# Kernel optimization log

Measured on AMD Instinct MI355X. Metric: run time of the kernel, lower is better.

## Reference

```python
import jax, jax.numpy as jnp
import numpy as np

B, T, K, D = 16, 1024, 8, 768
H = D // 2

def setup_inputs() -> dict:
    key = jax.random.key(0)
    ks = jax.random.split(key, 18)
    s = 0.02  # param init scale
    return {
        'emb':        jax.random.normal(ks[0], (B, T, D), jnp.float32),
        'cls_embed':  jax.random.normal(ks[1], (D,), jnp.float32),
        'Wg_w':       jax.random.normal(ks[2], (D, D), jnp.float32) * s,
        'Wg_b':       jax.random.normal(ks[3], (D,), jnp.float32) * s,
        'alpha_left': jax.random.normal(ks[4], (D,), jnp.float32),
        'alpha_right':jax.random.normal(ks[5], (D,), jnp.float32),
        'gru_Wih':    jax.random.normal(ks[6], (3 * H, D), jnp.float32) * s,
        'gru_bih':    jax.random.normal(ks[7], (3 * H,), jnp.float32) * s,
        'gru_Whh':    jax.random.normal(ks[8], (3 * H, H), jnp.float32) * s,
        'gru_bhh':    jax.random.normal(ks[9], (3 * H,), jnp.float32) * s,
        'Wc_w':       jax.random.normal(ks[10], (3, D + H), jnp.float32) * s,
        'Wc_b':       jax.random.normal(ks[11], (3,), jnp.float32) * s,
        'We_w':       jax.random.normal(ks[12], (3, D + H), jnp.float32) * s,
        'We_b':       jax.random.normal(ks[13], (3,), jnp.float32) * s,
        'child_idx':  jax.random.randint(ks[14], (B, T, K), 0, T, jnp.int32),
        'child_mask': jax.random.randint(ks[15], (B, T, K), 0, 2, jnp.int32),
        'clue_mask':  jax.random.randint(ks[16], (B, T), 0, 2, jnp.int32),
    }

def _forward(emb, cls_embed, Wg_w, Wg_b, alpha_left, alpha_right,
             gru_Wih, gru_bih, gru_Whh, gru_bhh, Wc_w, Wc_b, We_w, We_b,
             child_idx, child_mask, clue_mask):
    # ---- GAT over syntactic children (graph_attention) ----
    Wg_t = emb @ Wg_w.T + Wg_b                                  # [B,T,D] = W_g(t)
    self_score = Wg_t @ alpha_left                              # [B,T]  alpha_left . W_g(t_i)
    gather = jax.vmap(lambda w, i: w[i])                        # per-sentence child gather
    Wg_child = gather(Wg_t, child_idx)                          # [B,T,K,D]
    child_score = Wg_child @ alpha_right                        # [B,T,K]
    mask = child_mask.astype(bool)
    s = jax.nn.leaky_relu(self_score[..., None] + child_score, negative_slope=0.2)
    s = jnp.where(mask, s, -1e9)
    a = jax.nn.softmax(s, axis=-1)
    a = jnp.where(mask, a, 0.0)
    attn = jnp.einsum('btk,btkd->btd', a, Wg_child)             # a_ij @ Wg_tks
    has_child = mask.any(-1)                                    # no children -> keep t_i
    new_emb = emb + jnp.where(has_child[..., None], attn, 0.0)  # t_i' = t_i + sum

    # ---- G_W with prepended CLS row ----
    cls = jnp.broadcast_to(cls_embed, (B, 1, D))
    G_W = jnp.concatenate([cls, new_emb], axis=1)               # [B,T+1,D]
    m = jnp.concatenate([jnp.ones((B, 1), bool), clue_mask.astype(bool)], axis=1)

    # ---- GRU over clue subsequence (masked state update == packed sequence) ----
    x_proj = G_W @ gru_Wih.T + gru_bih                          # [B,T+1,3H]
    def cell(h, inp):
        xp, mt = inp                                            # [B,3H], [B]
        hp = h @ gru_Whh.T + gru_bhh
        xr, xz, xn = jnp.split(xp, 3, axis=-1)
        hr, hz, hn = jnp.split(hp, 3, axis=-1)
        r = jax.nn.sigmoid(xr + hr)
        z = jax.nn.sigmoid(xz + hz)
        n = jnp.tanh(xn + r * hn)
        h_new = (1.0 - z) * n + z * h
        h = jnp.where(mt[:, None], h_new, h)
        return h, None
    h0 = jnp.zeros((B, H), emb.dtype)
    h_clue, _ = jax.lax.scan(cell, h0, (x_proj.transpose(1, 0, 2), m.T))  # [B,H]

    # ---- cause / effect heads, drop CLS row ----
    feat = jnp.concatenate([G_W, jnp.broadcast_to(h_clue[:, None, :], (B, T + 1, H))], axis=-1)
    O_cause = (feat @ Wc_w.T + Wc_b)[:, 1:]                     # [B,T,3]
    O_effect = (feat @ We_w.T + We_b)[:, 1:]                    # [B,T,3]
    return O_cause, O_effect

def reference(emb, cls_embed, Wg_w, Wg_b, alpha_left, alpha_right,
              gru_Wih, gru_bih, gru_Whh, gru_bhh, Wc_w, Wc_b, We_w, We_b,
              child_idx, child_mask, clue_mask):
    return _forward(emb, cls_embed, Wg_w, Wg_b, alpha_left, alpha_right,
                    gru_Wih, gru_bih, gru_Whh, gru_bhh, Wc_w, Wc_b, We_w, We_b,
                    child_idx, child_mask, clue_mask)
```

## Files before the change

### kernel.cpp

```cpp
#include <hip/hip_runtime.h>
#include <hip/hip_bf16.h>
#include <math.h>

#define DD 768
#define HH 384
#define BB 16
#define TT 1024
#define NIH 1152
#define GSP 6

typedef __attribute__((ext_vector_type(8))) short short8;
typedef __attribute__((ext_vector_type(8))) __bf16 bf16x8;
typedef __attribute__((ext_vector_type(4))) float f32x4;

static __device__ __forceinline__ unsigned short f2bf(float f) {
  unsigned u = __float_as_uint(f);
  u += 0x7fffu + ((u >> 16) & 1u);
  return (unsigned short)(u >> 16);
}
static __device__ __forceinline__ float bf2f(unsigned short h) {
  return __uint_as_float(((unsigned)h) << 16);
}

__global__ void prep_convert(const float* __restrict__ wgw, const float* __restrict__ wih,
                             const float* __restrict__ whh,
                             unsigned short* __restrict__ wgw_bf, unsigned short* __restrict__ wih_bf,
                             unsigned short* __restrict__ whh_bf)
{
  const int n1 = DD*DD, n2 = NIH*DD, n3 = NIH*HH;
  int stride = gridDim.x * 256;
  for (int idx = blockIdx.x*256 + threadIdx.x; idx < n1+n2+n3; idx += stride) {
    if (idx < n1)            wgw_bf[idx]       = f2bf(wgw[idx]);
    else if (idx < n1+n2)    wih_bf[idx-n1]    = f2bf(wih[idx-n1]);
    else                     whh_bf[idx-n1-n2] = f2bf(whh[idx-n1-n2]);
  }
}

__global__ void prep_vecs(const float* __restrict__ wgw, const float* __restrict__ wgb,
                          const float* __restrict__ aL, const float* __restrict__ aR,
                          float* __restrict__ vLR, float* __restrict__ c01)
{
  int tid = threadIdx.x;
  if (blockIdx.x < 3) {
    int j = blockIdx.x*256 + tid;
    float al = 0.f, ar = 0.f;
    for (int i = 0; i < DD; ++i) { float wv = wgw[i*DD + j]; al += wv*aL[i]; ar += wv*aR[i]; }
    vLR[j] = al; vLR[DD + j] = ar;
  } else {
    float al = 0.f, ar = 0.f;
    for (int i = tid; i < DD; i += 256) { float bv = wgb[i]; al += bv*aL[i]; ar += bv*aR[i]; }
    for (int off = 32; off; off >>= 1) { al += __shfl_down(al, off); ar += __shfl_down(ar, off); }
    __shared__ float red[8];
    int w = tid >> 6, l = tid & 63;
    if (l == 0) { red[w*2] = al; red[w*2+1] = ar; }
    __syncthreads();
    if (tid == 0) { c01[0] = red[0]+red[2]+red[4]+red[6]; c01[1] = red[1]+red[3]+red[5]+red[7]; }
  }
}

__global__ __launch_bounds__(256) void scores_cvt(const float* __restrict__ emb,
    const float* __restrict__ vLR, const float* __restrict__ c01,
    float* __restrict__ ss, float* __restrict__ sr)
{
  int row = blockIdx.x, tid = threadIdx.x;
  const float* er = emb + (size_t)row*DD;
  float al = 0.f, ar = 0.f;
  for (int d = tid; d < DD; d += 256) {
    float e = er[d];
    al += e*vLR[d]; ar += e*vLR[DD+d];
  }
  for (int off = 32; off; off >>= 1) { al += __shfl_down(al, off); ar += __shfl_down(ar, off); }
  __shared__ float red[8];
  int w = tid >> 6, l = tid & 63;
  if (l == 0) { red[w*2] = al; red[w*2+1] = ar; }
  __syncthreads();
  if (tid == 0) {
    ss[row] = red[0]+red[2]+red[4]+red[6] + c01[0];
    sr[row] = red[1]+red[3]+red[5]+red[7] + c01[1];
  }
}

template<bool AF32>
__global__ __launch_bounds__(256) void gemm_bt(const void* __restrict__ Av,
    const unsigned short* __restrict__ Bw, const float* __restrict__ bias,
    unsigned short* __restrict__ C, int N, int MT, int Mreal)
{
  __shared__ __align__(16) unsigned short As[128][40];
  __shared__ __align__(16) unsigned short Bs[128][40];
  int tid = threadIdx.x;
  int tm = blockIdx.x % MT, tn = blockIdx.x / MT;
  int l = tid & 63, lr = l & 15, lk = l >> 4;
  int w = tid >> 6;
  int wm = (w >> 1)*64, wn = (w & 1)*64;
  f32x4 acc[4][4] = {};

  int c0 = tid, c1 = tid + 256;
  int r0 = c0 >> 2, ch0 = c0 & 3;
  int r1 = c1 >> 2, ch1 = c1 & 3;
  const unsigned short* Bbase = Bw + (size_t)tn*128*DD;

  for (int kt = 0; kt < 24; ++kt) {
    short8 va0, va1;
    if constexpr (AF32) {
      const float* Af = (const float*)Av + (size_t)tm*128*DD;
      f32x4 a0l = *(const f32x4*)(Af + r0*DD + kt*32 + ch0*8);
      f32x4 a0h = *(const f32x4*)(Af + r0*DD + kt*32 + ch0*8 + 4);
      f32x4 a1l = *(const f32x4*)(Af + r1*DD + kt*32 + ch1*8);
      f32x4 a1h = *(const f32x4*)(Af + r1*DD + kt*32 + ch1*8 + 4);
      #pragma unroll
      for (int j = 0; j < 4; ++j) {
        va0[j] = (short)f2bf(a0l[j]); va0[4+j] = (short)f2bf(a0h[j]);
        va1[j] = (short)f2bf(a1l[j]); va1[4+j] = (short)f2bf(a1h[j]);
      }
    } else {
      const unsigned short* Ab = (const unsigned short*)Av + (size_t)tm*128*DD;
      va0 = *(const short8*)(Ab + r0*DD + kt*32 + ch0*8);
      va1 = *(const short8*)(Ab + r1*DD + kt*32 + ch1*8);
    }
    short8 vb0 = *(const short8*)(Bbase + r0*DD + kt*32 + ch0*8);
    short8 vb1 = *(const short8*)(Bbase + r1*DD + kt*32 + ch1*8);
    __syncthreads();
    *(short8*)&As[r0][ch0*8] = va0;
    *(short8*)&As[r1][ch1*8] = va1;
    *(short8*)&Bs[r0][ch0*8] = vb0;
    *(short8*)&Bs[r1][ch1*8] = vb1;
    __syncthreads();
    bf16x8 af[4], bfr[4];
    #pragma unroll
    for (int mi = 0; mi < 4; ++mi)
      af[mi] = __builtin_bit_cast(bf16x8, *(const short8*)&As[wm + mi*16 + lr][lk*8]);
    #pragma unroll
    for (int ni = 0; ni < 4; ++ni)
      bfr[ni] = __builtin_bit_cast(bf16x8, *(const short8*)&Bs[wn + ni*16 + lr][lk*8]);
    #pragma unroll
    for (int mi = 0; mi < 4; ++mi)
      #pragma unroll
      for (int ni = 0; ni < 4; ++ni)
        acc[mi][ni] = __builtin_amdgcn_mfma_f32_16x16x32_bf16(af[mi], bfr[ni], acc[mi][ni], 0, 0, 0);
  }
  for (int mi = 0; mi < 4; ++mi) {
    int rbase = tm*128 + wm + mi*16 + lk*4;
    for (int ni = 0; ni < 4; ++ni) {
      int col = tn*128 + wn + ni*16 + lr;
      float bv = bias[col];
      #pragma unroll
      for (int jr = 0; jr < 4; ++jr) {
        int row = rbase + jr;
        if (row < Mreal) C[(size_t)row*N + col] = f2bf(acc[mi][ni][jr] + bv);
      }
    }
  }
}

__global__ __launch_bounds__(256) void gat_attn(const float* __restrict__ emb,
    const float* __restrict__ cls, const unsigned short* __restrict__ wgt_bf,
    const float* __restrict__ ss, const float* __restrict__ sr,
    const int* __restrict__ cidx, const int* __restrict__ cmask,
    unsigned short* __restrict__ gw_bf)
{
  int bx = blockIdx.x, tid = threadIdx.x;
  if (bx >= BB*TT) {
    int b = bx - BB*TT;
    unsigned short* dst = gw_bf + (size_t)(b*(TT+1))*DD;
    for (int d = tid; d < DD; d += 256) dst[d] = f2bf(cls[d]);
    return;
  }
  int b = bx >> 10, t = bx & 1023;
  __shared__ float sw[8];
  __shared__ int   si[8];
  __shared__ int   sm[8];
  if (tid < 8) {
    int ci = cidx[(size_t)bx*8 + tid];
    int cm = cmask[(size_t)bx*8 + tid];
    float s = ss[bx] + sr[(b<<10) + ci];
    s = s > 0.f ? s : 0.2f*s;
    sw[tid] = cm ? s : -1e9f;
    si[tid] = ci;
    sm[tid] = cm;
  }
  __syncthreads();
  float a[8];
  float mx = -1e30f;
  #pragma unroll
  for (int k = 0; k < 8; ++k) mx = fmaxf(mx, sw[k]);
  float sum = 0.f;
  #pragma unroll
  for (int k = 0; k < 8; ++k) { a[k] = expf(sw[k]-mx); sum += a[k]; }
  float inv = 1.f/sum;
  #pragma unroll
  for (int k = 0; k < 8; ++k) a[k] = sm[k] ? a[k]*inv : 0.f;
  const float* er = emb + (size_t)bx*DD;
  unsigned short* dst = gw_bf + (size_t)(b*(TT+1) + t + 1)*DD;
  for (int d = tid; d < DD; d += 256) {
    float acc = er[d];
    #pragma unroll
    for (int k = 0; k < 8; ++k)
      if (a[k] != 0.f) acc += a[k]*bf2f(wgt_bf[((size_t)(b<<10) + si[k])*DD + d]);
    dst[d] = f2bf(acc);
  }
}

__global__ __launch_bounds__(384, 2) void gru_scan(const unsigned short* __restrict__ whh_bf,
    const float* __restrict__ bhh, const unsigned short* __restrict__ xp,
    const int* __restrict__ clue, unsigned* __restrict__ hbuf,
    float* __restrict__ hfinal)
{
  __shared__ __align__(16) unsigned short h_bf[HH];
  __shared__ __align__(16) float y_s[192];
  __shared__ float bhh_s[192];
  __shared__ unsigned char m_s[TT+1];
  int tid = threadIdx.x;
  int b = blockIdx.x % BB, g = blockIdx.x / BB;
  int w = tid >> 6, l = tid & 63, lr = l & 15, lk = l >> 4;

  bf16x8 areg[2][12];
  #pragma unroll
  for (int i = 0; i < 2; ++i) {
    int rg = w*2 + i;
    int gate = rg >> 2;
    const unsigned short* src = whh_bf + (size_t)(gate*HH + g*64 + (rg & 3)*16 + lr)*HH;
    #pragma unroll
    for (int c = 0; c < 12; ++c) {
      int kt = 2*g + c; if (kt >= 12) kt -= 12;
      areg[i][c] = __builtin_bit_cast(bf16x8, *(const short8*)(src + kt*32 + lk*8));
    }
  }
  if (tid < 192) {
    int gate = tid / 64, e = tid % 64;
    bhh_s[tid] = bhh[gate*HH + g*64 + e];
  }
  h_bf[tid] = 0;
  for (int t = tid; t < TT; t += 384) m_s[t+1] = (clue[b*TT + t] != 0) ? 1 : 0;
  if (tid == 0) m_s[0] = 1;
  __syncthreads();

  float h_prev = 0.f;
  int gi = g*64 + tid;
  int s = 0;
  int rj = 0;
  if (tid >= 64) { int e = g*64 + 64 + (tid - 64); if (e >= HH) e -= HH; rj = e; }
  for (int t = 0; t <= TT; ++t) {
    if (!m_s[t]) continue;
    ++s;
    float xr = 0.f, xz = 0.f, xn = 0.f;
    if (tid < 64) {
      const unsigned short* xrow = xp + (size_t)(b*(TT+1) + t)*NIH;
      xr = bf2f(xrow[gi]); xz = bf2f(xrow[HH + gi]); xn = bf2f(xrow[2*HH + gi]);
    }
    f32x4 aco[2] = {};
    #pragma unroll
    for (int c = 0; c < 2; ++c) {
      bf16x8 bfr = __builtin_bit_cast(bf16x8, *(const short8*)&h_bf[g*64 + c*32 + lk*8]);
      #pragma unroll
      for (int i = 0; i < 2; ++i)
        aco[i] = __builtin_amdgcn_mfma_f32_16x16x32_bf16(areg[i][c], bfr, aco[i], 0, 0, 0);
    }
    if (s > 1 && tid >= 64) {
      const unsigned* pa = hbuf + ((size_t)(s-1)*BB + b)*HH + rj;
      unsigned tag = (unsigned)(s-1);
      unsigned v = __hip_atomic_load(pa, __ATOMIC_RELAXED, __HIP_MEMORY_SCOPE_AGENT);
      while ((v & 0xFFFFu) != tag)
        v = __hip_atomic_load(pa, __ATOMIC_RELAXED, __HIP_MEMORY_SCOPE_AGENT);
      h_bf[rj] = (unsigned short)(v >> 16);
    }
    __syncthreads();
    f32x4 acA[2] = {}, acB[2] = {};
    #pragma unroll
    for (int c = 2; c < 7; ++c) {
      int kk = g*64 + c*32; if (kk >= HH) kk -= HH;
      bf16x8 bfr = __builtin_bit_cast(bf16x8, *(const short8*)&h_bf[kk + lk*8]);
      #pragma unroll
      for (int i = 0; i < 2; ++i)
        acA[i] = __builtin_amdgcn_mfma_f32_16x16x32_bf16(areg[i][c], bfr, acA[i], 0, 0, 0);
    }
    #pragma unroll
    for (int c = 7; c < 12; ++c) {
      int kk = g*64 + c*32; if (kk >= HH) kk -= HH;
      bf16x8 bfr = __builtin_bit_cast(bf16x8, *(const short8*)&h_bf[kk + lk*8]);
      #pragma unroll
      for (int i = 0; i < 2; ++i)
        acB[i] = __builtin_amdgcn_mfma_f32_16x16x32_bf16(areg[i][c], bfr, acB[i], 0, 0, 0);
    }
    if (lr == 0) {
      #pragma unroll
      for (int i = 0; i < 2; ++i)
        *(f32x4*)&y_s[(w*2+i)*16 + lk*4] = aco[i] + acA[i] + acB[i];
    }
    __syncthreads();
    unsigned* slot = hbuf + ((size_t)s*BB + b)*HH;
    if (tid < 64) {
      float hr = y_s[tid]       + bhh_s[tid];
      float hz = y_s[64 + tid]  + bhh_s[64 + tid];
      float hn = y_s[128 + tid] + bhh_s[128 + tid];
      float rg = 1.f/(1.f + __expf(-(xr + hr)));
      float zg = 1.f/(1.f + __expf(-(xz + hz)));
      float a  = xn + rg*hn;
      a = fminf(fmaxf(a, -15.f), 15.f);
      float e2 = __expf(-2.f*a);
      float ng = (1.f - e2)/(1.f + e2);
      float hnew = (1.f - zg)*ng + zg*h_prev;
      h_prev = hnew;
      unsigned short hb16 = f2bf(hnew);
      h_bf[gi] = hb16;
      __hip_atomic_store(slot + gi, ((unsigned)hb16 << 16) | (unsigned)s,
                         __ATOMIC_RELAXED, __HIP_MEMORY_SCOPE_AGENT);
    }
    __syncthreads();
  }
  if (tid < 64) hfinal[b*HH + gi] = h_prev;
}

__global__ __launch_bounds__(384) void hpart_k(const float* __restrict__ hfinal,
    const float* __restrict__ Wc, const float* __restrict__ Wcb,
    const float* __restrict__ We, const float* __restrict__ Web, float* __restrict__ hpart)
{
  int b = blockIdx.x, tid = threadIdx.x;
  int j = tid >> 6, l = tid & 63;
  const float* wr = ((j < 3) ? (Wc + j*NIH) : (We + (j-3)*NIH)) + DD;
  float acc = 0.f;
  #pragma unroll
  for (int i = 0; i < 6; ++i) acc += hfinal[b*HH + l + i*64] * wr[l + i*64];
  for (int off = 32; off; off >>= 1) acc += __shfl_down(acc, off);
  if (l == 0) hpart[b*6 + j] = acc + ((j < 3) ? Wcb[j] : Web[j-3]);
}

__global__ __launch_bounds__(256) void heads(const unsigned short* __restrict__ gw_bf,
    const float* __restrict__ Wc, const float* __restrict__ We,
    const float* __restrict__ hpart, float* __restrict__ out)
{
  __shared__ float Wl[6][DD];
  int tid = threadIdx.x;
  for (int idx = tid; idx < 6*DD; idx += 256) {
    int j = idx / DD, d = idx % DD;
    Wl[j][d] = (j < 3) ? Wc[j*NIH + d] : We[(j-3)*NIH + d];
  }
  __syncthreads();
  int w = tid >> 6, l = tid & 63;
  int row = blockIdx.x*4 + w;
  int b = row >> 10, t = row & 1023;
  const unsigned short* gr = gw_bf + (size_t)(b*(TT+1) + t + 1)*DD;
  float acc[6] = {0,0,0,0,0,0};
  for (int i = 0; i < 12; ++i) {
    int d = l + i*64;
    float v = bf2f(gr[d]);
    #pragma unroll
    for (int j = 0; j < 6; ++j) acc[j] += v * Wl[j][d];
  }
  #pragma unroll
  for (int j = 0; j < 6; ++j)
    for (int off = 32; off; off >>= 1) acc[j] += __shfl_down(acc[j], off);
  if (l == 0) {
    const float* hp = hpart + b*6;
    float* oc = out + (size_t)b*TT*3 + t*3;
    float* oe = out + (size_t)BB*TT*3 + (size_t)b*TT*3 + t*3;
    oc[0] = acc[0]+hp[0]; oc[1] = acc[1]+hp[1]; oc[2] = acc[2]+hp[2];
    oe[0] = acc[3]+hp[3]; oe[1] = acc[4]+hp[4]; oe[2] = acc[5]+hp[5];
  }
}

extern "C" void kernel_launch(void* const* d_in, const int* in_sizes, int n_in,
                              void* d_out, int out_size, void* d_ws, size_t ws_size,
                              hipStream_t stream)
{
  const float* emb  = (const float*)d_in[0];
  const float* cls  = (const float*)d_in[1];
  const float* wgw  = (const float*)d_in[2];
  const float* wgb  = (const float*)d_in[3];
  const float* aL   = (const float*)d_in[4];
  const float* aR   = (const float*)d_in[5];
  const float* wih  = (const float*)d_in[6];
  const float* bih  = (const float*)d_in[7];
  const float* whh  = (const float*)d_in[8];
  const float* bhh  = (const float*)d_in[9];
  const float* wcw  = (const float*)d_in[10];
  const float* wcb  = (const float*)d_in[11];
  const float* wew  = (const float*)d_in[12];
  const float* web  = (const float*)d_in[13];
  const int* cidx   = (const int*)d_in[14];
  const int* cmask  = (const int*)d_in[15];
  const int* clue   = (const int*)d_in[16];
  (void)in_sizes; (void)n_in; (void)out_size; (void)ws_size;

  char* ws = (char*)d_ws;
  size_t off = 0;
  auto alloc = [&](size_t bytes) { char* p = ws + off; off += (bytes + 255) & ~(size_t)255; return p; };
  unsigned short* xp_bf  = (unsigned short*)alloc((size_t)16512*1152*2);
  unsigned short* wgt_bf = xp_bf;
  unsigned short* gw_bf  = (unsigned short*)alloc((size_t)16512*768*2);
  unsigned short* wgw_bf = (unsigned short*)alloc((size_t)768*768*2);
  unsigned short* wih_bf = (unsigned short*)alloc((size_t)1152*768*2);
  unsigned short* whh_bf = (unsigned short*)alloc((size_t)1152*384*2);
  float* vLR   = (float*)alloc(1536*4);
  float* c01   = (float*)alloc(256);
  float* ss    = (float*)alloc(16384*4);
  float* sr    = (float*)alloc(16384*4);
  unsigned* hbuf = (unsigned*)alloc((size_t)(TT+2)*BB*HH*4);
  float* hfin  = (float*)alloc((size_t)16*384*4);
  float* hpart = (float*)alloc(512);

  prep_convert<<<2048, 256, 0, stream>>>(wgw, wih, whh, wgw_bf, wih_bf, whh_bf);
  prep_vecs<<<4, 256, 0, stream>>>(wgw, wgb, aL, aR, vLR, c01);
  scores_cvt<<<16384, 256, 0, stream>>>(emb, vLR, c01, ss, sr);
  gemm_bt<true><<<128*6, 256, 0, stream>>>(emb, wgw_bf, wgb, wgt_bf, 768, 128, 16384);
  gat_attn<<<16384+16, 256, 0, stream>>>(emb, cls, wgt_bf, ss, sr, cidx, cmask, gw_bf);
  gemm_bt<false><<<129*9, 256, 0, stream>>>(gw_bf, wih_bf, bih, xp_bf, 1152, 129, 16400);
  gru_scan<<<BB*GSP, 384, 0, stream>>>(whh_bf, bhh, xp_bf, clue, hbuf, hfin);
  hpart_k<<<16, 384, 0, stream>>>(hfin, wcw, wcb, wew, web, hpart);
  heads<<<4096, 256, 0, stream>>>(gw_bf, wcw, wew, hpart, (float*)d_out);
}
```

Baseline: 839.4 us.

## Split GRU scan across 12 blocks per sequence with 32 hidden units each

```diff
diff --git a/kernel.cpp b/kernel.cpp
--- a/kernel.cpp
+++ b/kernel.cpp
@@ -7,7 +7,7 @@
 #define BB 16
 #define TT 1024
 #define NIH 1152
-#define GSP 6
+#define GSP 12
 
 typedef __attribute__((ext_vector_type(8))) short short8;
 typedef __attribute__((ext_vector_type(8))) __bf16 bf16x8;
@@ -206,28 +206,25 @@
     float* __restrict__ hfinal)
 {
   __shared__ __align__(16) unsigned short h_bf[HH];
-  __shared__ __align__(16) float y_s[192];
-  __shared__ float bhh_s[192];
+  __shared__ __align__(16) float y_s[96];
+  __shared__ float bhh_s[96];
   __shared__ unsigned char m_s[TT+1];
   int tid = threadIdx.x;
   int b = blockIdx.x % BB, g = blockIdx.x / BB;
   int w = tid >> 6, l = tid & 63, lr = l & 15, lk = l >> 4;
 
-  bf16x8 areg[2][12];
-  #pragma unroll
-  for (int i = 0; i < 2; ++i) {
-    int rg = w*2 + i;
-    int gate = rg >> 2;
-    const unsigned short* src = whh_bf + (size_t)(gate*HH + g*64 + (rg & 3)*16 + lr)*HH;
+  bf16x8 areg[12];
+  {
+    const unsigned short* src = whh_bf + (size_t)((w>>1)*HH + g*32 + (w&1)*16 + lr)*HH;
     #pragma unroll
     for (int c = 0; c < 12; ++c) {
-      int kt = 2*g + c; if (kt >= 12) kt -= 12;
-      areg[i][c] = __builtin_bit_cast(bf16x8, *(const short8*)(src + kt*32 + lk*8));
-    }
-  }
-  if (tid < 192) {
-    int gate = tid / 64, e = tid % 64;
-    bhh_s[tid] = bhh[gate*HH + g*64 + e];
+      int kt = g + c; if (kt >= 12) kt -= 12;
+      areg[c] = __builtin_bit_cast(bf16x8, *(const short8*)(src + kt*32 + lk*8));
+    }
+  }
+  if (tid < 96) {
+    int gate = tid >> 5, e = tid & 31;
+    bhh_s[tid] = bhh[gate*HH + g*32 + e];
   }
   h_bf[tid] = 0;
   for (int t = tid; t < TT; t += 384) m_s[t+1] = (clue[b*TT + t] != 0) ? 1 : 0;
@@ -235,27 +232,24 @@
   __syncthreads();
 
   float h_prev = 0.f;
-  int gi = g*64 + tid;
+  int gi = g*32 + tid;
   int s = 0;
   int rj = 0;
-  if (tid >= 64) { int e = g*64 + 64 + (tid - 64); if (e >= HH) e -= HH; rj = e; }
+  if (tid >= 32) { int e = g*32 + 32 + (tid - 32); if (e >= HH) e -= HH; rj = e; }
   for (int t = 0; t <= TT; ++t) {
     if (!m_s[t]) continue;
     ++s;
     float xr = 0.f, xz = 0.f, xn = 0.f;
-    if (tid < 64) {
+    if (tid < 32) {
       const unsigned short* xrow = xp + (size_t)(b*(TT+1) + t)*NIH;
       xr = bf2f(xrow[gi]); xz = bf2f(xrow[HH + gi]); xn = bf2f(xrow[2*HH + gi]);
     }
-    f32x4 aco[2] = {};
-    #pragma unroll
-    for (int c = 0; c < 2; ++c) {
-      bf16x8 bfr = __builtin_bit_cast(bf16x8, *(const short8*)&h_bf[g*64 + c*32 + lk*8]);
-      #pragma unroll
-      for (int i = 0; i < 2; ++i)
-        aco[i] = __builtin_amdgcn_mfma_f32_16x16x32_bf16(areg[i][c], bfr, aco[i], 0, 0, 0);
-    }
-    if (s > 1 && tid >= 64) {
+    f32x4 aco = {};
+    {
+      bf16x8 bfr = __builtin_bit_cast(bf16x8, *(const short8*)&h_bf[g*32 + lk*8]);
+      aco = __builtin_amdgcn_mfma_f32_16x16x32_bf16(areg[0], bfr, aco, 0, 0, 0);
+    }
+    if (s > 1 && tid >= 32) {
       const unsigned* pa = hbuf + ((size_t)(s-1)*BB + b)*HH + rj;
       unsigned tag = (unsigned)(s-1);
       unsigned v = __hip_atomic_load(pa, __ATOMIC_RELAXED, __HIP_MEMORY_SCOPE_AGENT);
@@ -264,34 +258,29 @@
       h_bf[rj] = (unsigned short)(v >> 16);
     }
     __syncthreads();
-    f32x4 acA[2] = {}, acB[2] = {};
-    #pragma unroll
-    for (int c = 2; c < 7; ++c) {
-      int kk = g*64 + c*32; if (kk >= HH) kk -= HH;
+    f32x4 acA = {}, acB = {};
+    #pragma unroll
+    for (int c = 1; c < 7; ++c) {
+      int kk = g*32 + c*32; if (kk >= HH) kk -= HH;
       bf16x8 bfr = __builtin_bit_cast(bf16x8, *(const short8*)&h_bf[kk + lk*8]);
-      #pragma unroll
-      for (int i = 0; i < 2; ++i)
-        acA[i] = __builtin_amdgcn_mfma_f32_16x16x32_bf16(areg[i][c], bfr, acA[i], 0, 0, 0);
+      acA = __builtin_amdgcn_mfma_f32_16x16x32_bf16(areg[c], bfr, acA, 0, 0, 0);
     }
     #pragma unroll
     for (int c = 7; c < 12; ++c) {
-      int kk = g*64 + c*32; if (kk >= HH) kk -= HH;
+      int kk = g*32 + c*32; if (kk >= HH) kk -= HH;
       bf16x8 bfr = __builtin_bit_cast(bf16x8, *(const short8*)&h_bf[kk + lk*8]);
-      #pragma unroll
-      for (int i = 0; i < 2; ++i)
-        acB[i] = __builtin_amdgcn_mfma_f32_16x16x32_bf16(areg[i][c], bfr, acB[i], 0, 0, 0);
+      acB = __builtin_amdgcn_mfma_f32_16x16x32_bf16(areg[c], bfr, acB, 0, 0, 0);
     }
     if (lr == 0) {
-      #pragma unroll
-      for (int i = 0; i < 2; ++i)
-        *(f32x4*)&y_s[(w*2+i)*16 + lk*4] = aco[i] + acA[i] + acB[i];
+      f32x4 ysum = aco + acA + acB;
+      *(f32x4*)&y_s[w*16 + lk*4] = ysum;
     }
     __syncthreads();
     unsigned* slot = hbuf + ((size_t)s*BB + b)*HH;
-    if (tid < 64) {
-      float hr = y_s[tid]       + bhh_s[tid];
-      float hz = y_s[64 + tid]  + bhh_s[64 + tid];
-      float hn = y_s[128 + tid] + bhh_s[128 + tid];
+    if (tid < 32) {
+      float hr = y_s[tid]      + bhh_s[tid];
+      float hz = y_s[32 + tid] + bhh_s[32 + tid];
+      float hn = y_s[64 + tid] + bhh_s[64 + tid];
       float rg = 1.f/(1.f + __expf(-(xr + hr)));
       float zg = 1.f/(1.f + __expf(-(xz + hz)));
       float a  = xn + rg*hn;
@@ -307,7 +296,7 @@
     }
     __syncthreads();
   }
-  if (tid < 64) hfinal[b*HH + gi] = h_prev;
+  if (tid < 32) hfinal[b*HH + gi] = h_prev;
 }
 
 __global__ __launch_bounds__(384) void hpart_k(const float* __restrict__ hfinal,
```

New measurement: 813.8 us. 3.0% less time.
